# Kernel optimization log

Hardware: AMD Instinct MI355X
Metric: run time of the kernel (lower is better)

Reference implementation:

```python
import jax, jax.numpy as jnp
import numpy as np

NUM_RBF = 16
MIN_MU = 2.0
MAX_MU = 22.0
K_NEIGHBORS = 48
MAX_REL = 32
POS_DIM = 16
EDGE_OUT = 128
N_TOKENS = 21
N_ATOMS = 14
N_ATOM_TYPES = 5  # N, CA, C, O + 1 virtual
W_NORMAL, W_B1, W_B2 = 0.58273431, -0.56802827, -0.54067466


def setup_inputs() -> dict:
    key = jax.random.key(0)
    ks = jax.random.split(key, 8)
    B, L = 2, 2048
    X = jax.random.normal(ks[0], (B, L, N_ATOMS, 3), jnp.float32) * 10.0
    X_m = jnp.ones((B, L, N_ATOMS), jnp.float32)
    S = jax.random.randint(ks[1], (B, L), 0, N_TOKENS)
    residue_idx = jnp.arange(B * L).reshape(B, L)
    mask = jnp.ones((B, L), jnp.float32)
    # token -> atom-slot index table for [N, CA, C, O] (per-token fancy indexing)
    table = jax.random.randint(ks[2], (N_TOKENS, 4), 0, N_ATOMS)
    n_pos_in = 2 * MAX_REL + 1
    W_pos = jax.random.normal(ks[3], (n_pos_in, POS_DIM), jnp.float32) * 0.05
    b_pos = jnp.zeros((POS_DIM,), jnp.float32)
    n_edge_in = POS_DIM + NUM_RBF * N_ATOM_TYPES * N_ATOM_TYPES  # 416
    W_e = jax.random.normal(ks[4], (n_edge_in, EDGE_OUT), jnp.float32) * 0.05
    ln_g = jnp.ones((EDGE_OUT,), jnp.float32)
    ln_b = jnp.zeros((EDGE_OUT,), jnp.float32)
    return {"X": X, "X_m": X_m, "S": S, "residue_idx": residue_idx, "mask": mask,
            "table": table, "W_pos": W_pos, "b_pos": b_pos, "W_e": W_e,
            "ln_g": ln_g, "ln_b": ln_b}


def _rbf(D):
    mu = jnp.linspace(MIN_MU, MAX_MU, NUM_RBF, dtype=D.dtype)
    sigma = (MAX_MU - MIN_MU) / NUM_RBF
    return jnp.exp(-jnp.square((D[..., None] - mu) / sigma))


def reference(X, X_m, S, residue_idx, mask, table, W_pos, b_pos, W_e, ln_g, ln_b):
    B, L = S.shape
    # token-dependent gather of backbone atoms [B,L,4,3]
    idx = table[S]
    X_bb = jnp.take_along_axis(X, idx[..., None], axis=2)
    N_, CA, C_ = X_bb[:, :, 0], X_bb[:, :, 1], X_bb[:, :, 2]
    # virtual atom (CB-like) from N, CA, C
    b1 = N_ - CA
    b2 = C_ - CA
    nrm = jnp.cross(b1, b2)
    Xv = W_NORMAL * nrm + W_B1 * b1 + W_B2 * b2 + CA
    X_all = jnp.concatenate([X_bb, Xv[:, :, None, :]], axis=2)  # [B,L,5,3]
    # pairwise CA distances + masked top-k neighbors
    diff = CA[:, :, None, :] - CA[:, None, :, :]
    D = jnp.sqrt(jnp.sum(diff * diff, -1) + 1e-6)
    m2 = mask[:, :, None] * mask[:, None, :]
    D_adj = D * m2 + (1.0 - m2) * 1e6
    _, E_idx = jax.lax.top_k(-D_adj, K_NEIGHBORS)  # [B,L,K]
    # gather neighbor atom coords [B,L,K,5,3]
    X_nb = jax.vmap(lambda xa, ei: xa[ei])(X_all, E_idx)
    d = X_all[:, :, None, :, None, :] - X_nb[:, :, :, None, :, :]  # [B,L,K,5,5,3]
    Dab = jnp.sqrt(jnp.sum(d * d, -1) + 1e-6)
    RBF = _rbf(Dab).reshape(B, L, K_NEIGHBORS, N_ATOM_TYPES * N_ATOM_TYPES * NUM_RBF)
    # positional encodings of relative residue offsets
    r_nb = jax.vmap(lambda r, ei: r[ei])(residue_idx, E_idx)
    off = jnp.clip(residue_idx[:, :, None] - r_nb + MAX_REL, 0, 2 * MAX_REL)
    pos = jax.nn.one_hot(off, 2 * MAX_REL + 1, dtype=RBF.dtype) @ W_pos + b_pos
    # edge embedding (no bias) + layernorm
    E = jnp.concatenate([pos, RBF], -1) @ W_e
    mu_ = jnp.mean(E, -1, keepdims=True)
    var = jnp.var(E, -1, keepdims=True)
    E = (E - mu_) * jax.lax.rsqrt(var + 1e-5) * ln_g + ln_b
    return E, E_idx
```

## Files before the change

### kernel.cpp

```cpp
#include <hip/hip_runtime.h>
#include <hip/hip_bf16.h>

#define Bq 2
#define Lq 2048
#define BLq (Bq*Lq)
#define KNB 48
#define NA 14
#define NTOK 21
#define NRBF 16
#define POSD 16
#define EOUT 128
#define KDIM 416
#define CSTRIDE 168
#define ESTRIDE 132
#define E_ELEMS (BLq*KNB*EOUT)

typedef __attribute__((ext_vector_type(8))) short short8;
typedef __attribute__((ext_vector_type(4))) float f32x4;

__device__ __forceinline__ unsigned short bf16_rn(float x) {
    unsigned int u = __float_as_uint(x);
    unsigned int r = (u + 0x7fffu + ((u >> 16) & 1u)) >> 16;
    return (unsigned short)r;
}

__global__ void prep_kernel(const float* __restrict__ X, const int* __restrict__ S,
                            const int* __restrict__ table, const float* __restrict__ mask,
                            const float* __restrict__ We,
                            float* __restrict__ Xall, float4* __restrict__ CA4,
                            short* __restrict__ Wp) {
    int bid = blockIdx.x;
    if (bid < 16) {
        int t = bid * 256 + threadIdx.x;
        if (t >= BLq) return;
        int s = S[t];
        float bb[4][3];
#pragma unroll
        for (int a = 0; a < 4; ++a) {
            int ia = table[s * 4 + a];
#pragma unroll
            for (int d = 0; d < 3; ++d) bb[a][d] = X[(t * NA + ia) * 3 + d];
        }
        float b1[3], b2[3], nr[3];
#pragma unroll
        for (int d = 0; d < 3; ++d) { b1[d] = bb[0][d] - bb[1][d]; b2[d] = bb[2][d] - bb[1][d]; }
        nr[0] = b1[1] * b2[2] - b1[2] * b2[1];
        nr[1] = b1[2] * b2[0] - b1[0] * b2[2];
        nr[2] = b1[0] * b2[1] - b1[1] * b2[0];
#pragma unroll
        for (int a = 0; a < 4; ++a)
#pragma unroll
            for (int d = 0; d < 3; ++d) Xall[t * 15 + a * 3 + d] = bb[a][d];
#pragma unroll
        for (int d = 0; d < 3; ++d) {
            float xv = 0.58273431f * nr[d] + (-0.56802827f) * b1[d] + (-0.54067466f) * b2[d] + bb[1][d];
            Xall[t * 15 + 12 + d] = xv;
        }
        CA4[t] = make_float4(bb[1][0], bb[1][1], bb[1][2], mask[t]);
    } else {
        int t = (bid - 16) * 256 + threadIdx.x;
        if (t >= 13 * 8 * 64 * 8) return;
        int j = t & 7;
        int lane = (t >> 3) & 63;
        int nt = (t >> 9) & 7;
        int kt = t >> 12;
        int k = kt * 32 + (lane >> 4) * 8 + j;
        int n = nt * 16 + (lane & 15);
        Wp[t] = (short)bf16_rn(We[k * 128 + n]);
    }
}

__global__ __launch_bounds__(256) void topk_kernel(const float4* __restrict__ CA4,
                                                   int* __restrict__ eidx_ws,
                                                   float* __restrict__ out_idx) {
    __shared__ unsigned int hist[2048];
    __shared__ unsigned long long buf[128];
    __shared__ unsigned int nacc;
    __shared__ unsigned int wtot[4];
    __shared__ int sh_bin, sh_excl, sh_cnt;

    int bl = blockIdx.x;
    int base = (bl >> 11) << 11;
    int tid = threadIdx.x;
    int lane = tid & 63;
    int w = tid >> 6;
    float4 q = CA4[bl];

    unsigned long long key[8];
#pragma unroll
    for (int i = 0; i < 8; ++i) {
        int j = tid + (i << 8);
        float4 c = CA4[base + j];
        float dx = __fsub_rn(q.x, c.x);
        float dy = __fsub_rn(q.y, c.y);
        float dz = __fsub_rn(q.z, c.z);
        float s = __fadd_rn(__fadd_rn(__fmul_rn(dx, dx), __fmul_rn(dy, dy)), __fmul_rn(dz, dz));
        float D = __fsqrt_rn(__fadd_rn(s, 1e-6f));
        float m2 = __fmul_rn(q.w, c.w);
        float Dadj = __fadd_rn(__fmul_rn(D, m2), __fmul_rn(__fsub_rn(1.0f, m2), 1000000.0f));
        key[i] = (((unsigned long long)__float_as_uint(Dadj)) << 16) | (unsigned int)j;
    }

    for (int i = tid; i < 2048; i += 256) hist[i] = 0;
    __syncthreads();
#pragma unroll
    for (int i = 0; i < 8; ++i) atomicAdd(&hist[(unsigned int)(key[i] >> 37)], 1u);
    __syncthreads();

    unsigned int loc[8], lsum = 0;
#pragma unroll
    for (int j = 0; j < 8; ++j) { loc[j] = hist[(tid << 3) + j]; lsum += loc[j]; }
    unsigned int incl = lsum;
#pragma unroll
    for (int o = 1; o < 64; o <<= 1) {
        unsigned int v = __shfl_up(incl, o);
        if (lane >= o) incl += v;
    }
    if (lane == 63) wtot[w] = incl;
    __syncthreads();
    unsigned int cum = incl - lsum;
#pragma unroll
    for (int u = 0; u < 4; ++u) cum += (u < w) ? wtot[u] : 0u;
#pragma unroll
    for (int j = 0; j < 8; ++j) {
        if ((int)cum < 48 && 48 <= (int)(cum + loc[j])) {
            sh_bin = (tid << 3) + j;
            sh_excl = (int)cum;
            sh_cnt = (int)loc[j];
        }
        cum += loc[j];
    }
    __syncthreads();

    unsigned long long prefix = (unsigned long long)(unsigned int)sh_bin;
    int need = 48 - sh_excl;
    int cnt = sh_cnt;
    int shift = 37;

    while (cnt > 80 && shift > 0) {
        shift = (shift >= 8) ? (shift - 8) : 0;
        hist[tid] = 0;
        __syncthreads();
#pragma unroll
        for (int i = 0; i < 8; ++i)
            if ((key[i] >> (shift + 8)) == prefix)
                atomicAdd(&hist[(unsigned int)((key[i] >> shift) & 255ull)], 1u);
        __syncthreads();
        if (tid < 64) {
            unsigned int h0 = hist[4 * tid + 0], h1 = hist[4 * tid + 1];
            unsigned int h2 = hist[4 * tid + 2], h3 = hist[4 * tid + 3];
            unsigned int s4 = h0 + h1 + h2 + h3;
            unsigned int incl2 = s4;
#pragma unroll
            for (int o = 1; o < 64; o <<= 1) {
                unsigned int v = __shfl_up(incl2, o);
                if (tid >= o) incl2 += v;
            }
            unsigned int excl2 = incl2 - s4;
            if ((int)excl2 < need && need <= (int)incl2) {
                unsigned int cb = excl2;
                unsigned int hh[4] = {h0, h1, h2, h3};
                int bsel = 3;
#pragma unroll
                for (int bb2 = 0; bb2 < 4; ++bb2) {
                    if ((int)(cb + hh[bb2]) >= need) { bsel = bb2; break; }
                    cb += hh[bb2];
                }
                sh_bin = 4 * tid + bsel;
                sh_excl = (int)cb;
                sh_cnt = (int)hh[bsel];
            }
        }
        __syncthreads();
        prefix = (prefix << 8) | (unsigned long long)(unsigned int)sh_bin;
        need -= sh_excl;
        cnt = sh_cnt;
    }

    if (tid == 0) nacc = 0;
    __syncthreads();
#pragma unroll
    for (int i = 0; i < 8; ++i) {
        bool p = (key[i] >> shift) <= prefix;
        unsigned long long m = __ballot(p);
        if (m != 0ull) {
            int leader = __ffsll((long long)m) - 1;
            unsigned int bpos = 0;
            if (lane == leader) bpos = atomicAdd(&nacc, (unsigned int)__popcll(m));
            bpos = (unsigned int)__shfl((int)bpos, leader);
            if (p) {
                unsigned int pos = bpos + (unsigned int)__popcll(m & ((1ull << lane) - 1ull));
                if (pos < 128) buf[pos] = key[i];
            }
        }
    }
    __syncthreads();
    unsigned int mcnt = nacc;
    if (mcnt > 128) mcnt = 128;
    if (tid < 128 && tid >= (int)mcnt) buf[tid] = ~0ULL;
    __syncthreads();

    int mp = (int)((mcnt + 7u) & ~7u);
    if (mp > 128) mp = 128;
    if (tid < 128) {
        unsigned long long k = buf[tid];
        int rank = 0;
        for (int u = 0; u < mp; ++u) rank += (buf[u] < k) ? 1 : 0;
        if (rank < KNB) {
            int j = (int)(k & 0xffffull);
            eidx_ws[bl * KNB + rank] = j;
            out_idx[bl * KNB + rank] = (float)j;
        }
    }
}

__global__ __launch_bounds__(256, 6) void edge_kernel(
    const float* __restrict__ Xall, const int* __restrict__ eidx_ws,
    const int* __restrict__ ridx, const float* __restrict__ Wpos,
    const float* __restrict__ bpos, const short* __restrict__ Wp,
    const float* __restrict__ lng, const float* __restrict__ lnb,
    float* __restrict__ out) {
    __shared__ __align__(16) char smem[25344];
    float* Dsm = (float*)smem;
    unsigned short* Asm = (unsigned short*)(smem + 4800);
    float* Xq = (float*)(smem + 20928);
    float* Xn = (float*)(smem + 20992);
    int* offs = (int*)(smem + 23872);
    float* Esm = (float*)smem;

    int bl = blockIdx.x;
    int b = bl >> 11;
    int tid = threadIdx.x;

    if (tid < KNB) {
        int j = eidx_ws[bl * KNB + tid];
        int off = ridx[bl] - ridx[(b << 11) + j] + 32;
        offs[tid] = min(max(off, 0), 64);
    }
    if (tid < 15) Xq[tid] = Xall[bl * 15 + tid];
    for (int f = tid; f < KNB * 15; f += 256) {
        int k = f / 15, d = f - k * 15;
        int j = eidx_ws[bl * KNB + k];
        Xn[f] = Xall[((b << 11) + j) * 15 + d];
    }
    __syncthreads();

    for (int f = tid; f < KNB * 25; f += 256) {
        int k = f / 25, p = f - k * 25;
        int a = p / 5, c = p - a * 5;
        float dx = Xq[a * 3 + 0] - Xn[k * 15 + c * 3 + 0];
        float dy = Xq[a * 3 + 1] - Xn[k * 15 + c * 3 + 1];
        float dz = Xq[a * 3 + 2] - Xn[k * 15 + c * 3 + 2];
        Dsm[f] = sqrtf(dx * dx + dy * dy + dz * dz + 1e-6f);
    }
    __syncthreads();

    int w = tid >> 6, lane = tid & 63;
    int quad = lane >> 4, lr = lane & 15;
    f32x4 acc[3][2];
#pragma unroll
    for (int mt = 0; mt < 3; ++mt)
#pragma unroll
        for (int nt = 0; nt < 2; ++nt) acc[mt][nt] = (f32x4){0.f, 0.f, 0.f, 0.f};

    auto rbf_rows = [&](int pr, int r0, int lc, int k0, int kn) {
        const float s1 = 0.96089795f;
        const float dlt = 1.28119727f;
        float c0 = (2.0f + 1.3333333f * (float)r0) * s1;
        for (int k = k0; k < k0 + kn; ++k) {
            float D = Dsm[k * 25 + pr];
            float u0 = __builtin_fmaf(D, s1, -c0);
            float u1 = u0 - dlt;
            float v0 = __builtin_amdgcn_exp2f(-(u0 * u0));
            float v1 = __builtin_amdgcn_exp2f(-(u1 * u1));
            *(__hip_bfloat162*)(Asm + k * CSTRIDE + lc) = __float22bfloat162_rn(make_float2(v0, v1));
        }
    };

    auto gemm_chunk = [&](int ktBase, int ktCnt) {
#pragma unroll
        for (int ktl = 0; ktl < ktCnt; ++ktl) {
            int kt = ktBase + ktl;
            short8 bf0 = *(const short8*)(Wp + (((kt * 8 + 2 * w + 0) * 64 + lane) << 3));
            short8 bf1 = *(const short8*)(Wp + (((kt * 8 + 2 * w + 1) * 64 + lane) << 3));
#pragma unroll
            for (int mt = 0; mt < 3; ++mt) {
                short8 af = *(const short8*)(&Asm[(mt * 16 + lr) * CSTRIDE + ktl * 32 + quad * 8]);
                acc[mt][0] = __builtin_amdgcn_mfma_f32_16x16x32_bf16(af, bf0, acc[mt][0], 0, 0, 0);
                acc[mt][1] = __builtin_amdgcn_mfma_f32_16x16x32_bf16(af, bf1, acc[mt][1], 0, 0, 0);
            }
        }
    };

    if (tid < 240) {
        int kseg = tid / 80, c2 = tid - kseg * 80;
        int k0 = kseg << 4;
        if (c2 < 8) {
            int cd = c2 << 1;
            float bp0 = bpos[cd], bp1 = bpos[cd + 1];
            for (int k = k0; k < k0 + 16; ++k) {
                int off = offs[k];
                float v0 = Wpos[off * 16 + cd] + bp0;
                float v1 = Wpos[off * 16 + cd + 1] + bp1;
                *(__hip_bfloat162*)(Asm + k * CSTRIDE + cd) = __float22bfloat162_rn(make_float2(v0, v1));
            }
        } else {
            int f2 = c2 - 8;
            rbf_rows(f2 >> 3, (f2 & 7) << 1, 16 + (f2 << 1), k0, 16);
        }
    }
    __syncthreads();
    gemm_chunk(0, 5);
    __syncthreads();

    {
        int kseg = tid >> 6, c2 = tid & 63;
        rbf_rows(9 + (c2 >> 3), (c2 & 7) << 1, c2 << 1, kseg * 12, 12);
    }
    __syncthreads();
    gemm_chunk(5, 4);
    __syncthreads();

    {
        int kseg = tid >> 6, c2 = tid & 63;
        rbf_rows(17 + (c2 >> 3), (c2 & 7) << 1, c2 << 1, kseg * 12, 12);
    }
    __syncthreads();
    gemm_chunk(9, 4);
    __syncthreads();

#pragma unroll
    for (int mt = 0; mt < 3; ++mt)
#pragma unroll
        for (int ntl = 0; ntl < 2; ++ntl) {
            int col = (2 * w + ntl) * 16 + lr;
#pragma unroll
            for (int r = 0; r < 4; ++r) {
                int row = mt * 16 + quad * 4 + r;
                Esm[row * ESTRIDE + col] = acc[mt][ntl][r];
            }
        }
    __syncthreads();

    float g0 = lng[lane], g1 = lng[lane + 64];
    float bb0 = lnb[lane], bb1 = lnb[lane + 64];
    for (int r = w; r < KNB; r += 4) {
        float v0 = Esm[r * ESTRIDE + lane];
        float v1 = Esm[r * ESTRIDE + lane + 64];
        float s = v0 + v1;
        float qq = __builtin_fmaf(v0, v0, v1 * v1);
#pragma unroll
        for (int o = 32; o > 0; o >>= 1) { s += __shfl_xor(s, o); qq += __shfl_xor(qq, o); }
        float mean = s * 0.0078125f;
        float var = __builtin_fmaf(-mean, mean, qq * 0.0078125f);
        float inv = rsqrtf(var + 1e-5f);
        float a0 = inv * g0, a1 = inv * g1;
        int ob = (bl * KNB + r) * EOUT;
        out[ob + lane] = __builtin_fmaf(v0 - mean, a0, bb0);
        out[ob + lane + 64] = __builtin_fmaf(v1 - mean, a1, bb1);
    }
}

extern "C" void kernel_launch(void* const* d_in, const int* in_sizes, int n_in,
                              void* d_out, int out_size, void* d_ws, size_t ws_size,
                              hipStream_t stream) {
    const float* X    = (const float*)d_in[0];
    const int*   S    = (const int*)d_in[2];
    const int*   ridx = (const int*)d_in[3];
    const float* mask = (const float*)d_in[4];
    const int*   tab  = (const int*)d_in[5];
    const float* Wpos = (const float*)d_in[6];
    const float* bpos = (const float*)d_in[7];
    const float* We   = (const float*)d_in[8];
    const float* lng  = (const float*)d_in[9];
    const float* lnb  = (const float*)d_in[10];
    float* out = (float*)d_out;

    char* ws = (char*)d_ws;
    float*  Xall = (float*)ws;
    int*    eidx = (int*)(ws + 245760);
    short*  Wp   = (short*)(ws + 245760 + 786432);
    float4* CA4  = (float4*)(ws + 245760 + 786432 + 106496);

    prep_kernel<<<224, 256, 0, stream>>>(X, S, tab, mask, We, Xall, CA4, Wp);
    topk_kernel<<<BLq, 256, 0, stream>>>(CA4, eidx, out + E_ELEMS);
    edge_kernel<<<BLq, 256, 0, stream>>>(Xall, eidx, ridx, Wpos, bpos, Wp, lng, lnb, out);
}
```

Before: 195.6 us.

## Fuse top-k selection into edge kernel and compute RBF via exponential recurrence

Merges the top-k neighbor selection kernel into the edge embedding kernel. Neighbor indices now stay in shared memory, which removes a launch and the global workspace round trip for indices. The radix histogram is reduced to 1024 bins with 4-way lane-replicated counters to cut atomic contention. The 16 RBF values per distance are now built from a few exp2 calls plus a multiplicative recurrence and written as packed bf16 vectors, instead of one exp2 per value. The trade-offs are higher shared-memory and register pressure in the fused kernel and slightly different rounding of the RBF values.

```diff
diff --git a/kernel.cpp b/kernel.cpp
--- a/kernel.cpp
+++ b/kernel.cpp
@@ -10,7 +10,6 @@
 #define NRBF 16
 #define POSD 16
 #define EOUT 128
-#define KDIM 416
 #define CSTRIDE 168
 #define ESTRIDE 132
 #define E_ELEMS (BLq*KNB*EOUT)
@@ -22,6 +21,12 @@
     unsigned int u = __float_as_uint(x);
     unsigned int r = (u + 0x7fffu + ((u >> 16) & 1u)) >> 16;
     return (unsigned short)r;
+}
+
+__device__ __forceinline__ unsigned int pkbf2(float a, float b) {
+    __hip_bfloat162 t = __float22bfloat162_rn(make_float2(a, b));
+    union { __hip_bfloat162 h; unsigned int u; } cv; cv.h = t;
+    return cv.u;
 }
 
 __global__ void prep_kernel(const float* __restrict__ X, const int* __restrict__ S,
@@ -70,22 +75,80 @@
     }
 }
 
-__global__ __launch_bounds__(256) void topk_kernel(const float4* __restrict__ CA4,
-                                                   int* __restrict__ eidx_ws,
-                                                   float* __restrict__ out_idx) {
-    __shared__ unsigned int hist[2048];
-    __shared__ unsigned long long buf[128];
-    __shared__ unsigned int nacc;
-    __shared__ unsigned int wtot[4];
+__device__ __forceinline__ void rbf16(float D, unsigned short* dst) {
+    const float s1   = 0.96089793f;
+    const float dlt  = 1.28119724f;
+    const float dlt2 = 1.64146638f;
+    const float tdl  = 2.56239448f;
+    const float Cg   = 0.10273972f;
+    float u0 = __builtin_fmaf(D, s1, -1.92179585f);
+    uint4 qa, qb;
+    {
+        float ua = u0 - 5.12478895f;
+        float va = __builtin_amdgcn_exp2f(-(ua * ua));
+        float eu = fminf(__builtin_fmaf(tdl, ua, -dlt2), 120.0f);
+        float ed = fminf(__builtin_fmaf(-tdl, ua, -dlt2), 120.0f);
+        float gu = __builtin_amdgcn_exp2f(eu);
+        float gd = __builtin_amdgcn_exp2f(ed);
+        float v4 = va;
+        float v5 = v4 * gu; float g2 = gu * Cg;
+        float v6 = v5 * g2;
+        float v7 = v6 * (g2 * Cg);
+        float v3 = v4 * gd; float h2 = gd * Cg;
+        float v2 = v3 * h2; float h3 = h2 * Cg;
+        float v1 = v2 * h3;
+        float v0 = v1 * (h3 * Cg);
+        qa.x = pkbf2(v0, v1); qa.y = pkbf2(v2, v3);
+        qa.z = pkbf2(v4, v5); qa.w = pkbf2(v6, v7);
+    }
+    {
+        float ub = u0 - 15.37436684f;
+        float vb = __builtin_amdgcn_exp2f(-(ub * ub));
+        float eu = fminf(__builtin_fmaf(tdl, ub, -dlt2), 120.0f);
+        float ed = fminf(__builtin_fmaf(-tdl, ub, -dlt2), 120.0f);
+        float gu = __builtin_amdgcn_exp2f(eu);
+        float gd = __builtin_amdgcn_exp2f(ed);
+        float v12 = vb;
+        float v13 = v12 * gu; float g2 = gu * Cg;
+        float v14 = v13 * g2;
+        float v15 = v14 * (g2 * Cg);
+        float v11 = v12 * gd; float h2 = gd * Cg;
+        float v10 = v11 * h2; float h3 = h2 * Cg;
+        float v9  = v10 * h3;
+        float v8  = v9 * (h3 * Cg);
+        qb.x = pkbf2(v8, v9);   qb.y = pkbf2(v10, v11);
+        qb.z = pkbf2(v12, v13); qb.w = pkbf2(v14, v15);
+    }
+    *(uint4*)dst = qa;
+    *(uint4*)(dst + 8) = qb;
+}
+
+__global__ __launch_bounds__(256, 6) void edge_kernel(
+    const float4* __restrict__ CA4, const float* __restrict__ Xall,
+    const int* __restrict__ ridx, const float* __restrict__ Wpos,
+    const float* __restrict__ bpos, const short* __restrict__ Wp,
+    const float* __restrict__ lng, const float* __restrict__ lnb,
+    float* __restrict__ out, float* __restrict__ out_idx) {
+    __shared__ __align__(16) char smem[25344];
+    unsigned int* histR = (unsigned int*)smem;
+    unsigned int* hist8 = (unsigned int*)smem;
+    unsigned long long* buf = (unsigned long long*)(smem + 16384);
+    float* Dsm = (float*)smem;
+    unsigned short* Asm = (unsigned short*)(smem + 4800);
+    float* Xq = (float*)(smem + 20928);
+    float* Xn = (float*)(smem + 20992);
+    int* offs = (int*)(smem + 23872);
+    int* eidxl = (int*)(smem + 24064);
+    float* Esm = (float*)smem;
+    __shared__ unsigned int nacc, wtot[4];
     __shared__ int sh_bin, sh_excl, sh_cnt;
 
     int bl = blockIdx.x;
     int base = (bl >> 11) << 11;
     int tid = threadIdx.x;
-    int lane = tid & 63;
-    int w = tid >> 6;
+    int w = tid >> 6, lane = tid & 63;
+
     float4 q = CA4[bl];
-
     unsigned long long key[8];
 #pragma unroll
     for (int i = 0; i < 8; ++i) {
@@ -101,15 +164,23 @@
         key[i] = (((unsigned long long)__float_as_uint(Dadj)) << 16) | (unsigned int)j;
     }
 
-    for (int i = tid; i < 2048; i += 256) hist[i] = 0;
-    __syncthreads();
-#pragma unroll
-    for (int i = 0; i < 8; ++i) atomicAdd(&hist[(unsigned int)(key[i] >> 37)], 1u);
-    __syncthreads();
-
-    unsigned int loc[8], lsum = 0;
-#pragma unroll
-    for (int j = 0; j < 8; ++j) { loc[j] = hist[(tid << 3) + j]; lsum += loc[j]; }
+    {
+        uint4 z = make_uint4(0u, 0u, 0u, 0u);
+        for (int i = tid; i < 1024; i += 256) ((uint4*)histR)[i] = z;
+    }
+    __syncthreads();
+#pragma unroll
+    for (int i = 0; i < 8; ++i)
+        atomicAdd(&histR[(((unsigned int)(key[i] >> 38)) << 2) | (unsigned int)(lane & 3)], 1u);
+    __syncthreads();
+
+    unsigned int loc[4], lsum = 0;
+#pragma unroll
+    for (int j = 0; j < 4; ++j) {
+        uint4 r4 = ((const uint4*)histR)[tid * 4 + j];
+        loc[j] = r4.x + r4.y + r4.z + r4.w;
+        lsum += loc[j];
+    }
     unsigned int incl = lsum;
 #pragma unroll
     for (int o = 1; o < 64; o <<= 1) {
@@ -122,9 +193,9 @@
 #pragma unroll
     for (int u = 0; u < 4; ++u) cum += (u < w) ? wtot[u] : 0u;
 #pragma unroll
-    for (int j = 0; j < 8; ++j) {
+    for (int j = 0; j < 4; ++j) {
         if ((int)cum < 48 && 48 <= (int)(cum + loc[j])) {
-            sh_bin = (tid << 3) + j;
+            sh_bin = tid * 4 + j;
             sh_excl = (int)cum;
             sh_cnt = (int)loc[j];
         }
@@ -135,20 +206,20 @@
     unsigned long long prefix = (unsigned long long)(unsigned int)sh_bin;
     int need = 48 - sh_excl;
     int cnt = sh_cnt;
-    int shift = 37;
+    int shift = 38;
 
     while (cnt > 80 && shift > 0) {
         shift = (shift >= 8) ? (shift - 8) : 0;
-        hist[tid] = 0;
+        hist8[tid] = 0;
         __syncthreads();
 #pragma unroll
         for (int i = 0; i < 8; ++i)
             if ((key[i] >> (shift + 8)) == prefix)
-                atomicAdd(&hist[(unsigned int)((key[i] >> shift) & 255ull)], 1u);
+                atomicAdd(&hist8[(unsigned int)((key[i] >> shift) & 255ull)], 1u);
         __syncthreads();
         if (tid < 64) {
-            unsigned int h0 = hist[4 * tid + 0], h1 = hist[4 * tid + 1];
-            unsigned int h2 = hist[4 * tid + 2], h3 = hist[4 * tid + 3];
+            unsigned int h0 = hist8[4 * tid + 0], h1 = hist8[4 * tid + 1];
+            unsigned int h2 = hist8[4 * tid + 2], h3 = hist8[4 * tid + 3];
             unsigned int s4 = h0 + h1 + h2 + h3;
             unsigned int incl2 = s4;
 #pragma unroll
@@ -185,11 +256,11 @@
         unsigned long long m = __ballot(p);
         if (m != 0ull) {
             int leader = __ffsll((long long)m) - 1;
-            unsigned int bpos = 0;
-            if (lane == leader) bpos = atomicAdd(&nacc, (unsigned int)__popcll(m));
-            bpos = (unsigned int)__shfl((int)bpos, leader);
+            unsigned int bp2 = 0;
+            if (lane == leader) bp2 = atomicAdd(&nacc, (unsigned int)__popcll(m));
+            bp2 = (unsigned int)__shfl((int)bp2, leader);
             if (p) {
-                unsigned int pos = bpos + (unsigned int)__popcll(m & ((1ull << lane) - 1ull));
+                unsigned int pos = bp2 + (unsigned int)__popcll(m & ((1ull << lane) - 1ull));
                 if (pos < 128) buf[pos] = key[i];
             }
         }
@@ -208,40 +279,22 @@
         for (int u = 0; u < mp; ++u) rank += (buf[u] < k) ? 1 : 0;
         if (rank < KNB) {
             int j = (int)(k & 0xffffull);
-            eidx_ws[bl * KNB + rank] = j;
+            eidxl[rank] = j;
             out_idx[bl * KNB + rank] = (float)j;
         }
     }
-}
-
-__global__ __launch_bounds__(256, 6) void edge_kernel(
-    const float* __restrict__ Xall, const int* __restrict__ eidx_ws,
-    const int* __restrict__ ridx, const float* __restrict__ Wpos,
-    const float* __restrict__ bpos, const short* __restrict__ Wp,
-    const float* __restrict__ lng, const float* __restrict__ lnb,
-    float* __restrict__ out) {
-    __shared__ __align__(16) char smem[25344];
-    float* Dsm = (float*)smem;
-    unsigned short* Asm = (unsigned short*)(smem + 4800);
-    float* Xq = (float*)(smem + 20928);
-    float* Xn = (float*)(smem + 20992);
-    int* offs = (int*)(smem + 23872);
-    float* Esm = (float*)smem;
-
-    int bl = blockIdx.x;
-    int b = bl >> 11;
-    int tid = threadIdx.x;
+    __syncthreads();
 
     if (tid < KNB) {
-        int j = eidx_ws[bl * KNB + tid];
-        int off = ridx[bl] - ridx[(b << 11) + j] + 32;
+        int j = eidxl[tid];
+        int off = ridx[bl] - ridx[base + j] + 32;
         offs[tid] = min(max(off, 0), 64);
     }
     if (tid < 15) Xq[tid] = Xall[bl * 15 + tid];
     for (int f = tid; f < KNB * 15; f += 256) {
         int k = f / 15, d = f - k * 15;
-        int j = eidx_ws[bl * KNB + k];
-        Xn[f] = Xall[((b << 11) + j) * 15 + d];
+        int j = eidxl[k];
+        Xn[f] = Xall[(base + j) * 15 + d];
     }
     __syncthreads();
 
@@ -255,27 +308,12 @@
     }
     __syncthreads();
 
-    int w = tid >> 6, lane = tid & 63;
     int quad = lane >> 4, lr = lane & 15;
     f32x4 acc[3][2];
 #pragma unroll
     for (int mt = 0; mt < 3; ++mt)
 #pragma unroll
         for (int nt = 0; nt < 2; ++nt) acc[mt][nt] = (f32x4){0.f, 0.f, 0.f, 0.f};
-
-    auto rbf_rows = [&](int pr, int r0, int lc, int k0, int kn) {
-        const float s1 = 0.96089795f;
-        const float dlt = 1.28119727f;
-        float c0 = (2.0f + 1.3333333f * (float)r0) * s1;
-        for (int k = k0; k < k0 + kn; ++k) {
-            float D = Dsm[k * 25 + pr];
-            float u0 = __builtin_fmaf(D, s1, -c0);
-            float u1 = u0 - dlt;
-            float v0 = __builtin_amdgcn_exp2f(-(u0 * u0));
-            float v1 = __builtin_amdgcn_exp2f(-(u1 * u1));
-            *(__hip_bfloat162*)(Asm + k * CSTRIDE + lc) = __float22bfloat162_rn(make_float2(v0, v1));
-        }
-    };
 
     auto gemm_chunk = [&](int ktBase, int ktCnt) {
 #pragma unroll
@@ -292,38 +330,40 @@
         }
     };
 
-    if (tid < 240) {
-        int kseg = tid / 80, c2 = tid - kseg * 80;
-        int k0 = kseg << 4;
-        if (c2 < 8) {
-            int cd = c2 << 1;
-            float bp0 = bpos[cd], bp1 = bpos[cd + 1];
-            for (int k = k0; k < k0 + 16; ++k) {
-                int off = offs[k];
-                float v0 = Wpos[off * 16 + cd] + bp0;
-                float v1 = Wpos[off * 16 + cd + 1] + bp1;
-                *(__hip_bfloat162*)(Asm + k * CSTRIDE + cd) = __float22bfloat162_rn(make_float2(v0, v1));
-            }
-        } else {
-            int f2 = c2 - 8;
-            rbf_rows(f2 >> 3, (f2 & 7) << 1, 16 + (f2 << 1), k0, 16);
-        }
+    if (tid < KNB) {
+        int off = offs[tid];
+        const float4* wr = (const float4*)(Wpos + off * 16);
+        const float4* bp = (const float4*)bpos;
+        float4 a0 = wr[0], a1 = wr[1], a2 = wr[2], a3 = wr[3];
+        float4 b0 = bp[0], b1 = bp[1], b2 = bp[2], b3 = bp[3];
+        uint4 o1, o2;
+        o1.x = pkbf2(a0.x + b0.x, a0.y + b0.y); o1.y = pkbf2(a0.z + b0.z, a0.w + b0.w);
+        o1.z = pkbf2(a1.x + b1.x, a1.y + b1.y); o1.w = pkbf2(a1.z + b1.z, a1.w + b1.w);
+        o2.x = pkbf2(a2.x + b2.x, a2.y + b2.y); o2.y = pkbf2(a2.z + b2.z, a2.w + b2.w);
+        o2.z = pkbf2(a3.x + b3.x, a3.y + b3.y); o2.w = pkbf2(a3.z + b3.z, a3.w + b3.w);
+        unsigned short* dst = Asm + tid * CSTRIDE;
+        *(uint4*)dst = o1;
+        *(uint4*)(dst + 8) = o2;
+    }
+    for (int it = tid; it < 9 * KNB; it += 256) {
+        int prl = it / KNB, k = it - prl * KNB;
+        rbf16(Dsm[k * 25 + prl], Asm + k * CSTRIDE + 16 + prl * 16);
     }
     __syncthreads();
     gemm_chunk(0, 5);
     __syncthreads();
 
-    {
-        int kseg = tid >> 6, c2 = tid & 63;
-        rbf_rows(9 + (c2 >> 3), (c2 & 7) << 1, c2 << 1, kseg * 12, 12);
+    for (int it = tid; it < 8 * KNB; it += 256) {
+        int prl = it / KNB, k = it - prl * KNB;
+        rbf16(Dsm[k * 25 + 9 + prl], Asm + k * CSTRIDE + prl * 16);
     }
     __syncthreads();
     gemm_chunk(5, 4);
     __syncthreads();
 
-    {
-        int kseg = tid >> 6, c2 = tid & 63;
-        rbf_rows(17 + (c2 >> 3), (c2 & 7) << 1, c2 << 1, kseg * 12, 12);
+    for (int it = tid; it < 8 * KNB; it += 256) {
+        int prl = it / KNB, k = it - prl * KNB;
+        rbf16(Dsm[k * 25 + 17 + prl], Asm + k * CSTRIDE + prl * 16);
     }
     __syncthreads();
     gemm_chunk(9, 4);
@@ -378,11 +418,10 @@
 
     char* ws = (char*)d_ws;
     float*  Xall = (float*)ws;
-    int*    eidx = (int*)(ws + 245760);
-    short*  Wp   = (short*)(ws + 245760 + 786432);
-    float4* CA4  = (float4*)(ws + 245760 + 786432 + 106496);
+    short*  Wp   = (short*)(ws + 245760);
+    float4* CA4  = (float4*)(ws + 245760 + 106496);
 
     prep_kernel<<<224, 256, 0, stream>>>(X, S, tab, mask, We, Xall, CA4, Wp);
-    topk_kernel<<<BLq, 256, 0, stream>>>(CA4, eidx, out + E_ELEMS);
-    edge_kernel<<<BLq, 256, 0, stream>>>(Xall, eidx, ridx, Wpos, bpos, Wp, lng, lnb, out);
-}
+    edge_kernel<<<BLq, 256, 0, stream>>>(CA4, Xall, ridx, Wpos, bpos, Wp, lng, lnb,
+                                         out, out + E_ELEMS);
+}
```

Result: faster. 183.2 us (-6.3%).
